# Kernel tuning notes

Hardware: AMD Instinct MI355X
Metric: run time of the kernel (lower is better)

The kernel has to match this reference:

```python
import jax, jax.numpy as jnp
import numpy as np

N_QUBITS = 6
N_LAYERS = 3
FEATURE_DIM = 512
ENC_HIDDEN = max(32, N_QUBITS * 4)  # 32
HEAD_HIDDEN = 128
G, T = 54, 24
DIM = 2 ** N_QUBITS  # 64


def _ry_batched(angles):
    # angles: [B] -> batched RY matrices [B, 2, 2] (complex64)
    c = jnp.cos(angles * 0.5)
    s = jnp.sin(angles * 0.5)
    U = jnp.stack([jnp.stack([c, -s], -1), jnp.stack([s, c], -1)], -2)
    return U.astype(jnp.complex64)


def _rot(phi, theta, omega):
    # PennyLane Rot = RZ(omega) RY(theta) RZ(phi); returns [2, 2] complex64
    c = jnp.cos(theta * 0.5).astype(jnp.complex64)
    s = jnp.sin(theta * 0.5).astype(jnp.complex64)
    ep = jnp.exp(-0.5j * (phi + omega).astype(jnp.complex64))  # e^{-i(phi+omega)/2}
    em = jnp.exp(-0.5j * (phi - omega).astype(jnp.complex64))  # e^{-i(phi-omega)/2}
    u00 = ep * c
    u01 = -jnp.conj(em) * s
    u10 = em * s
    u11 = jnp.conj(ep) * c
    return jnp.stack([jnp.stack([u00, u01]), jnp.stack([u10, u11])])


def _apply_1q_batched(state, U, q):
    # state: [B, 2^n]; U: [B, 2, 2] (per-sample gate, e.g. data-encoding RY)
    B = state.shape[0]
    st = state.reshape(B, 2 ** q, 2, -1)
    st = jnp.einsum('bij,bljr->blir', U, st)
    return st.reshape(B, -1)


def _apply_1q(state, U, q):
    # state: [B, 2^n]; U: [2, 2] shared across batch (trainable Rot)
    B = state.shape[0]
    st = state.reshape(B, 2 ** q, 2, -1)
    st = jnp.einsum('ij,bljr->blir', U, st)
    return st.reshape(B, -1)


def _apply_cnot(state, c, t):
    # state: [B, 2^n]; flip target axis where control bit == 1
    B = state.shape[0]
    st = state.reshape((B,) + (2,) * N_QUBITS)
    ax_c, ax_t = 1 + c, 1 + t
    s0 = jnp.take(st, 0, axis=ax_c)
    s1 = jnp.take(st, 1, axis=ax_c)
    s1 = jnp.flip(s1, axis=ax_t if ax_t < ax_c else ax_t - 1)
    st = jnp.stack([s0, s1], axis=ax_c)
    return st.reshape(B, -1)


def _expvals_z(state):
    # <Z_q> for every qubit: [B, n]
    B = state.shape[0]
    probs = (state.real ** 2 + state.imag ** 2).reshape((B,) + (2,) * N_QUBITS)
    outs = []
    for q in range(N_QUBITS):
        axes = tuple(i for i in range(1, N_QUBITS + 1) if i != q + 1)
        p = probs.sum(axes)  # [B, 2]
        outs.append(p[:, 0] - p[:, 1])
    return jnp.stack(outs, -1)


def _circuit(angles, q_weights):
    # angles: [B, n_qubits] float32; q_weights: [L, n, 3]
    B = angles.shape[0]
    state = jnp.zeros((B, DIM), jnp.complex64).at[:, 0].set(1.0)
    for layer in range(N_LAYERS):
        # data_reuploading=True -> re-encode every layer
        for q in range(N_QUBITS):
            state = _apply_1q_batched(state, _ry_batched(angles[:, q]), q)
        for q in range(N_QUBITS):
            w = q_weights[layer, q]
            state = _apply_1q(state, _rot(w[0], w[1], w[2]), q)
        for q in range(0, N_QUBITS - 1, 2):
            state = _apply_cnot(state, q, q + 1)
        for q in range(1, N_QUBITS - 1, 2):
            state = _apply_cnot(state, q, q + 1)
        state = _apply_cnot(state, N_QUBITS - 1, 0)  # n_qubits > 2
    return _expvals_z(state)


def setup_inputs() -> dict:
    key = jax.random.key(0)
    ks = jax.random.split(key, 10)
    B = 32768
    return {
        'x': jax.random.normal(ks[0], (B, FEATURE_DIM), jnp.float32),
        'enc_w1': 0.05 * jax.random.normal(ks[1], (FEATURE_DIM, ENC_HIDDEN), jnp.float32),
        'enc_b1': jnp.zeros((ENC_HIDDEN,), jnp.float32),
        'enc_w2': 0.05 * jax.random.normal(ks[2], (ENC_HIDDEN, N_QUBITS), jnp.float32),
        'enc_b2': jnp.zeros((N_QUBITS,), jnp.float32),
        'q_weights': 0.01 * jax.random.normal(ks[3], (N_LAYERS, N_QUBITS, 3), jnp.float32),
        'head_w1': 0.1 * jax.random.normal(ks[4], (N_QUBITS, HEAD_HIDDEN), jnp.float32),
        'head_b1': jnp.zeros((HEAD_HIDDEN,), jnp.float32),
        'head_w2': 0.05 * jax.random.normal(ks[5], (HEAD_HIDDEN, G * T), jnp.float32),
        'head_b2': jnp.zeros((G * T,), jnp.float32),
    }


def reference(x, enc_w1, enc_b1, enc_w2, enc_b2, q_weights,
              head_w1, head_b1, head_w2, head_b2):
    # classical encoder -> angles [B, n_qubits]
    h = jnp.tanh(x @ enc_w1 + enc_b1)
    angles = h @ enc_w2 + enc_b2
    # batched state-vector PQC simulation
    z = _circuit(angles, q_weights).astype(jnp.float32)  # [B, n_qubits]
    # classical head (dropout is identity in eval)
    g = jax.nn.relu(z @ head_w1 + head_b1)
    logits = g @ head_w2 + head_b2
    return logits.reshape(-1, G, T)
```

## Files before the change

kernel.cpp:

```cpp
#include <hip/hip_runtime.h>

typedef __bf16 bf16x8 __attribute__((ext_vector_type(8)));
typedef float floatx4 __attribute__((ext_vector_type(4)));
typedef unsigned short ushort8 __attribute__((ext_vector_type(8)));

__device__ __forceinline__ unsigned short f2bf(float f) {
    unsigned u = __float_as_uint(f);
    u += 0x7fffu + ((u >> 16) & 1u);
    return (unsigned short)(u >> 16);
}

__global__ __launch_bounds__(256) void prep_kernel(
    const float* __restrict__ w2, const float* __restrict__ qw,
    unsigned short* __restrict__ w2t, float* __restrict__ umat) {
    int t = blockIdx.x * 256 + threadIdx.x;
    if (t < 18) {
        float phi = qw[t * 3], theta = qw[t * 3 + 1], omega = qw[t * 3 + 2];
        float c = cosf(0.5f * theta), s = sinf(0.5f * theta);
        float po = 0.5f * (phi + omega), pm = 0.5f * (phi - omega);
        float epr = cosf(po), epi = -sinf(po);
        float emr = cosf(pm), emi = -sinf(pm);
        float* u = umat + t * 8;
        u[0] = epr * c;  u[1] = epi * c;
        u[2] = -emr * s; u[3] = emi * s;
        u[4] = emr * s;  u[5] = emi * s;
        u[6] = epr * c;  u[7] = -epi * c;
    }
    int nn = t >> 4;
    int kc = (t & 15) * 8;
    if (nn < 1296) {
        ushort8 pk;
#pragma unroll
        for (int j = 0; j < 8; ++j) pk[j] = f2bf(w2[(size_t)(kc + j) * 1296 + nn]);
        *(ushort8*)(w2t + (size_t)nn * 128 + kc) = pk;
    }
}

__global__ __launch_bounds__(256) void enc_kernel(
    const float* __restrict__ x, const float* __restrict__ w1,
    const float* __restrict__ b1, const float* __restrict__ w2,
    const float* __restrict__ b2, float* __restrict__ angles) {
    __shared__ float part[4][64][33];
    __shared__ float hsh[64][33];
    int lane = threadIdx.x & 63;
    int wave = threadIdx.x >> 6;
    int swave = __builtin_amdgcn_readfirstlane(wave);
    size_t row = (size_t)blockIdx.x * 64 + lane;
    const float2* x2 = (const float2*)(x + row * 512 + swave * 128);
    const float* wseg = w1 + swave * 128 * 32;

    float acc[32];
#pragma unroll
    for (int j = 0; j < 32; ++j) acc[j] = 0.f;

#pragma clang loop unroll(disable)
    for (int k2 = 0; k2 < 64; ++k2) {
        float2 xv = x2[k2];
        const float* wr = wseg + k2 * 64;
#pragma unroll
        for (int j = 0; j < 32; ++j) acc[j] = fmaf(wr[j], xv.x, acc[j]);
#pragma unroll
        for (int j = 0; j < 32; ++j) acc[j] = fmaf(wr[32 + j], xv.y, acc[j]);
    }
#pragma unroll
    for (int j = 0; j < 32; ++j) part[wave][lane][j] = acc[j];
    __syncthreads();

    int rl = threadIdx.x & 63;
    int jg = (threadIdx.x >> 6) * 8;
#pragma unroll
    for (int jj = 0; jj < 8; ++jj) {
        int j = jg + jj;
        float v = part[0][rl][j] + part[1][rl][j] + part[2][rl][j] + part[3][rl][j] + b1[j];
        hsh[rl][j] = tanhf(v);
    }
    __syncthreads();

    if (threadIdx.x < 64) {
        float h[32];
#pragma unroll
        for (int j = 0; j < 32; ++j) h[j] = hsh[threadIdx.x][j];
#pragma unroll
        for (int q = 0; q < 6; ++q) {
            float a = b2[q];
#pragma unroll
            for (int j = 0; j < 32; ++j) a = fmaf(h[j], w2[j * 6 + q], a);
            angles[((size_t)blockIdx.x * 64 + threadIdx.x) * 6 + q] = a;
        }
    }
}

template <int ST>
__device__ __forceinline__ void apply_g(float* sr, float* si,
    float m00r, float m00i, float m01r, float m01i,
    float m10r, float m10i, float m11r, float m11i) {
#pragma unroll
    for (int i = 0; i < 64; ++i) {
        if ((i & ST) == 0) {
            int i1 = i + ST;
            float r0 = sr[i], u0 = si[i], r1 = sr[i1], u1 = si[i1];
            sr[i]  = m00r * r0 - m00i * u0 + m01r * r1 - m01i * u1;
            si[i]  = m00r * u0 + m00i * r0 + m01r * u1 + m01i * r1;
            sr[i1] = m10r * r0 - m10i * u0 + m11r * r1 - m11i * u1;
            si[i1] = m10r * u0 + m10i * r0 + m11r * u1 + m11i * r1;
        }
    }
}

template <int CB, int TB>
__device__ __forceinline__ void cnot_g(float* sr, float* si) {
#pragma unroll
    for (int i = 0; i < 64; ++i) {
        if ((i & CB) && !(i & TB)) {
            int i1 = i + TB;
            float tr = sr[i]; sr[i] = sr[i1]; sr[i1] = tr;
            float ti = si[i]; si[i] = si[i1]; si[i1] = ti;
        }
    }
}

__global__ __launch_bounds__(64) void quantum_kernel(
    const float* __restrict__ angles, const float* __restrict__ umat,
    const float* __restrict__ hw1, const float* __restrict__ hb1,
    unsigned short* __restrict__ g) {
    int s = blockIdx.x * 64 + threadIdx.x;
    float ca[6], sa[6];
#pragma unroll
    for (int q = 0; q < 6; ++q) {
        float a = 0.5f * angles[(size_t)s * 6 + q];
        ca[q] = cosf(a);
        sa[q] = sinf(a);
    }
    float sr[64], si[64];
#pragma unroll
    for (int i = 0; i < 64; ++i) { sr[i] = 0.f; si[i] = 0.f; }
    sr[0] = 1.f;

#pragma clang loop unroll(disable)
    for (int layer = 0; layer < 3; ++layer) {
        const float* ub = umat + layer * 48;
#define DOQ(Q, ST) {                                                      \
        const float* u = ub + (Q) * 8;                                    \
        float c = ca[Q], ss = sa[Q];                                      \
        float m00r = u[0] * c + u[2] * ss, m00i = u[1] * c + u[3] * ss;   \
        float m01r = u[2] * c - u[0] * ss, m01i = u[3] * c - u[1] * ss;   \
        float m10r = u[4] * c + u[6] * ss, m10i = u[5] * c + u[7] * ss;   \
        float m11r = u[6] * c - u[4] * ss, m11i = u[7] * c - u[5] * ss;   \
        apply_g<ST>(sr, si, m00r, m00i, m01r, m01i, m10r, m10i, m11r, m11i); }
        DOQ(0, 32) DOQ(1, 16) DOQ(2, 8) DOQ(3, 4) DOQ(4, 2) DOQ(5, 1)
#undef DOQ
        cnot_g<32, 16>(sr, si);
        cnot_g<8, 4>(sr, si);
        cnot_g<2, 1>(sr, si);
        cnot_g<16, 8>(sr, si);
        cnot_g<4, 2>(sr, si);
        cnot_g<1, 32>(sr, si);
    }

    float z[6] = {0.f, 0.f, 0.f, 0.f, 0.f, 0.f};
#pragma unroll
    for (int i = 0; i < 64; ++i) {
        float p = sr[i] * sr[i] + si[i] * si[i];
        z[0] += (i & 32) ? -p : p;
        z[1] += (i & 16) ? -p : p;
        z[2] += (i & 8)  ? -p : p;
        z[3] += (i & 4)  ? -p : p;
        z[4] += (i & 2)  ? -p : p;
        z[5] += (i & 1)  ? -p : p;
    }

    unsigned short* gp = g + (size_t)s * 128;
#pragma unroll 2
    for (int j0 = 0; j0 < 128; j0 += 8) {
        ushort8 pk;
#pragma unroll
        for (int jj = 0; jj < 8; ++jj) {
            int j = j0 + jj;
            float a = hb1[j];
#pragma unroll
            for (int q = 0; q < 6; ++q) a = fmaf(z[q], hw1[q * 128 + j], a);
            a = fmaxf(a, 0.f);
            pk[jj] = f2bf(a);
        }
        *(ushort8*)(gp + j0) = pk;
    }
}

__global__ __launch_bounds__(256) void head_gemm(
    const unsigned short* __restrict__ g, const unsigned short* __restrict__ w2t,
    const float* __restrict__ b2, float* __restrict__ out) {
    int lane = threadIdx.x & 63;
    int task = blockIdx.x * 4 + (threadIdx.x >> 6);
    int m = task / 27;
    int n = task - m * 27;
    int row0 = m * 64, col0 = n * 48;
    int l15 = lane & 15, quad = lane >> 4;

    const unsigned short* ap = w2t + (size_t)(col0 + l15) * 128 + quad * 8;
    const unsigned short* bp = g + (size_t)(row0 + l15) * 128 + quad * 8;

    floatx4 acc[12];
#pragma unroll
    for (int i = 0; i < 12; ++i) acc[i] = (floatx4)0.f;

#pragma unroll
    for (int ks = 0; ks < 4; ++ks) {
        bf16x8 af[3], bf[4];
#pragma unroll
        for (int t = 0; t < 3; ++t) af[t] = *(const bf16x8*)(ap + (size_t)t * 16 * 128 + ks * 32);
#pragma unroll
        for (int sub = 0; sub < 4; ++sub) bf[sub] = *(const bf16x8*)(bp + (size_t)sub * 16 * 128 + ks * 32);
#pragma unroll
        for (int t = 0; t < 3; ++t)
#pragma unroll
            for (int sub = 0; sub < 4; ++sub)
                acc[t * 4 + sub] = __builtin_amdgcn_mfma_f32_16x16x32_bf16(af[t], bf[sub], acc[t * 4 + sub], 0, 0, 0);
    }

#pragma unroll
    for (int t = 0; t < 3; ++t) {
        const float* bb = b2 + col0 + t * 16 + quad * 4;
        floatx4 bias = { bb[0], bb[1], bb[2], bb[3] };
#pragma unroll
        for (int sub = 0; sub < 4; ++sub) {
            floatx4 v = acc[t * 4 + sub] + bias;
            floatx4* dst = (floatx4*)(out + (size_t)(row0 + sub * 16 + l15) * 1296 + col0 + t * 16 + quad * 4);
            __builtin_nontemporal_store(v, dst);
        }
    }
}

extern "C" void kernel_launch(void* const* d_in, const int* in_sizes, int n_in,
                              void* d_out, int out_size, void* d_ws, size_t ws_size,
                              hipStream_t stream) {
    const float* x   = (const float*)d_in[0];
    const float* ew1 = (const float*)d_in[1];
    const float* eb1 = (const float*)d_in[2];
    const float* ew2 = (const float*)d_in[3];
    const float* eb2 = (const float*)d_in[4];
    const float* qw  = (const float*)d_in[5];
    const float* hw1 = (const float*)d_in[6];
    const float* hb1 = (const float*)d_in[7];
    const float* hw2 = (const float*)d_in[8];
    const float* hb2 = (const float*)d_in[9];
    float* out = (float*)d_out;

    char* ws = (char*)d_ws;
    unsigned short* g   = (unsigned short*)(ws);
    unsigned short* w2t = (unsigned short*)(ws + 8388608);
    float* angles       = (float*)(ws + 8720384);
    float* umat         = (float*)(ws + 9506816);

    prep_kernel<<<dim3(81), dim3(256), 0, stream>>>(hw2, qw, w2t, umat);
    enc_kernel<<<dim3(512), dim3(256), 0, stream>>>(x, ew1, eb1, ew2, eb2, angles);
    quantum_kernel<<<dim3(512), dim3(64), 0, stream>>>(angles, umat, hw1, hb1, g);
    head_gemm<<<dim3(3456), dim3(256), 0, stream>>>(g, w2t, hb2, out);
}
```

Before: 318.6 us.

## Fuse prep, encoder and quantum kernels into one front kernel

```diff
diff --git a/kernel.cpp b/kernel.cpp
--- a/kernel.cpp
+++ b/kernel.cpp
@@ -8,86 +8,6 @@
     unsigned u = __float_as_uint(f);
     u += 0x7fffu + ((u >> 16) & 1u);
     return (unsigned short)(u >> 16);
-}
-
-__global__ __launch_bounds__(256) void prep_kernel(
-    const float* __restrict__ w2, const float* __restrict__ qw,
-    unsigned short* __restrict__ w2t, float* __restrict__ umat) {
-    int t = blockIdx.x * 256 + threadIdx.x;
-    if (t < 18) {
-        float phi = qw[t * 3], theta = qw[t * 3 + 1], omega = qw[t * 3 + 2];
-        float c = cosf(0.5f * theta), s = sinf(0.5f * theta);
-        float po = 0.5f * (phi + omega), pm = 0.5f * (phi - omega);
-        float epr = cosf(po), epi = -sinf(po);
-        float emr = cosf(pm), emi = -sinf(pm);
-        float* u = umat + t * 8;
-        u[0] = epr * c;  u[1] = epi * c;
-        u[2] = -emr * s; u[3] = emi * s;
-        u[4] = emr * s;  u[5] = emi * s;
-        u[6] = epr * c;  u[7] = -epi * c;
-    }
-    int nn = t >> 4;
-    int kc = (t & 15) * 8;
-    if (nn < 1296) {
-        ushort8 pk;
-#pragma unroll
-        for (int j = 0; j < 8; ++j) pk[j] = f2bf(w2[(size_t)(kc + j) * 1296 + nn]);
-        *(ushort8*)(w2t + (size_t)nn * 128 + kc) = pk;
-    }
-}
-
-__global__ __launch_bounds__(256) void enc_kernel(
-    const float* __restrict__ x, const float* __restrict__ w1,
-    const float* __restrict__ b1, const float* __restrict__ w2,
-    const float* __restrict__ b2, float* __restrict__ angles) {
-    __shared__ float part[4][64][33];
-    __shared__ float hsh[64][33];
-    int lane = threadIdx.x & 63;
-    int wave = threadIdx.x >> 6;
-    int swave = __builtin_amdgcn_readfirstlane(wave);
-    size_t row = (size_t)blockIdx.x * 64 + lane;
-    const float2* x2 = (const float2*)(x + row * 512 + swave * 128);
-    const float* wseg = w1 + swave * 128 * 32;
-
-    float acc[32];
-#pragma unroll
-    for (int j = 0; j < 32; ++j) acc[j] = 0.f;
-
-#pragma clang loop unroll(disable)
-    for (int k2 = 0; k2 < 64; ++k2) {
-        float2 xv = x2[k2];
-        const float* wr = wseg + k2 * 64;
-#pragma unroll
-        for (int j = 0; j < 32; ++j) acc[j] = fmaf(wr[j], xv.x, acc[j]);
-#pragma unroll
-        for (int j = 0; j < 32; ++j) acc[j] = fmaf(wr[32 + j], xv.y, acc[j]);
-    }
-#pragma unroll
-    for (int j = 0; j < 32; ++j) part[wave][lane][j] = acc[j];
-    __syncthreads();
-
-    int rl = threadIdx.x & 63;
-    int jg = (threadIdx.x >> 6) * 8;
-#pragma unroll
-    for (int jj = 0; jj < 8; ++jj) {
-        int j = jg + jj;
-        float v = part[0][rl][j] + part[1][rl][j] + part[2][rl][j] + part[3][rl][j] + b1[j];
-        hsh[rl][j] = tanhf(v);
-    }
-    __syncthreads();
-
-    if (threadIdx.x < 64) {
-        float h[32];
-#pragma unroll
-        for (int j = 0; j < 32; ++j) h[j] = hsh[threadIdx.x][j];
-#pragma unroll
-        for (int q = 0; q < 6; ++q) {
-            float a = b2[q];
-#pragma unroll
-            for (int j = 0; j < 32; ++j) a = fmaf(h[j], w2[j * 6 + q], a);
-            angles[((size_t)blockIdx.x * 64 + threadIdx.x) * 6 + q] = a;
-        }
-    }
 }
 
 template <int ST>
@@ -119,18 +39,95 @@
     }
 }
 
-__global__ __launch_bounds__(64) void quantum_kernel(
-    const float* __restrict__ angles, const float* __restrict__ umat,
+__global__ __launch_bounds__(256) void fused_front(
+    const float* __restrict__ x, const float* __restrict__ w1,
+    const float* __restrict__ b1, const float* __restrict__ w2,
+    const float* __restrict__ b2, const float* __restrict__ qw,
     const float* __restrict__ hw1, const float* __restrict__ hb1,
-    unsigned short* __restrict__ g) {
-    int s = blockIdx.x * 64 + threadIdx.x;
+    const float* __restrict__ hw2,
+    unsigned short* __restrict__ w2t, unsigned short* __restrict__ g) {
+
+    if (blockIdx.x >= 512) {
+        int t = (blockIdx.x - 512) * 256 + threadIdx.x;
+        int nn = t >> 4;
+        int kc = (t & 15) * 8;
+        if (nn < 1296) {
+            ushort8 pk;
+#pragma unroll
+            for (int j = 0; j < 8; ++j) pk[j] = f2bf(hw2[(size_t)(kc + j) * 1296 + nn]);
+            *(ushort8*)(w2t + (size_t)nn * 128 + kc) = pk;
+        }
+        return;
+    }
+
+    __shared__ float part[4][64][33];
+    __shared__ float hsh[64][33];
+    __shared__ float umat_s[144];
+
+    if (threadIdx.x < 18) {
+        int t = threadIdx.x;
+        float phi = qw[t * 3], theta = qw[t * 3 + 1], omega = qw[t * 3 + 2];
+        float c = cosf(0.5f * theta), s = sinf(0.5f * theta);
+        float po = 0.5f * (phi + omega), pm = 0.5f * (phi - omega);
+        float epr = cosf(po), epi = -sinf(po);
+        float emr = cosf(pm), emi = -sinf(pm);
+        float* u = umat_s + t * 8;
+        u[0] = epr * c;  u[1] = epi * c;
+        u[2] = -emr * s; u[3] = emi * s;
+        u[4] = emr * s;  u[5] = emi * s;
+        u[6] = epr * c;  u[7] = -epi * c;
+    }
+
+    int lane = threadIdx.x & 63;
+    int wave = threadIdx.x >> 6;
+    int swave = __builtin_amdgcn_readfirstlane(wave);
+    size_t row = (size_t)blockIdx.x * 64 + lane;
+    const float2* x2 = (const float2*)(x + row * 512 + swave * 128);
+    const float* wseg = w1 + swave * 128 * 32;
+
+    float acc[32];
+#pragma unroll
+    for (int j = 0; j < 32; ++j) acc[j] = 0.f;
+
+#pragma clang loop unroll(disable)
+    for (int k2 = 0; k2 < 64; ++k2) {
+        float2 xv = x2[k2];
+        const float* wr = wseg + k2 * 64;
+#pragma unroll
+        for (int j = 0; j < 32; ++j) acc[j] = fmaf(wr[j], xv.x, acc[j]);
+#pragma unroll
+        for (int j = 0; j < 32; ++j) acc[j] = fmaf(wr[32 + j], xv.y, acc[j]);
+    }
+#pragma unroll
+    for (int j = 0; j < 32; ++j) part[wave][lane][j] = acc[j];
+    __syncthreads();
+
+    int rl = threadIdx.x & 63;
+    int jg = (threadIdx.x >> 6) * 8;
+#pragma unroll
+    for (int jj = 0; jj < 8; ++jj) {
+        int j = jg + jj;
+        float v = part[0][rl][j] + part[1][rl][j] + part[2][rl][j] + part[3][rl][j] + b1[j];
+        hsh[rl][j] = tanhf(v);
+    }
+    __syncthreads();
+
+    if (threadIdx.x >= 64) return;
+
+    float h[32];
+#pragma unroll
+    for (int j = 0; j < 32; ++j) h[j] = hsh[threadIdx.x][j];
     float ca[6], sa[6];
 #pragma unroll
     for (int q = 0; q < 6; ++q) {
-        float a = 0.5f * angles[(size_t)s * 6 + q];
+        float a = b2[q];
+#pragma unroll
+        for (int j = 0; j < 32; ++j) a = fmaf(h[j], w2[j * 6 + q], a);
+        a = 0.5f * a;
         ca[q] = cosf(a);
         sa[q] = sinf(a);
     }
+
     float sr[64], si[64];
 #pragma unroll
     for (int i = 0; i < 64; ++i) { sr[i] = 0.f; si[i] = 0.f; }
@@ -138,7 +135,7 @@
 
 #pragma clang loop unroll(disable)
     for (int layer = 0; layer < 3; ++layer) {
-        const float* ub = umat + layer * 48;
+        const float* ub = umat_s + layer * 48;
 #define DOQ(Q, ST) {                                                      \
         const float* u = ub + (Q) * 8;                                    \
         float c = ca[Q], ss = sa[Q];                                      \
@@ -169,6 +166,7 @@
         z[5] += (i & 1)  ? -p : p;
     }
 
+    int s = blockIdx.x * 64 + threadIdx.x;
     unsigned short* gp = g + (size_t)s * 128;
 #pragma unroll 2
     for (int j0 = 0; j0 < 128; j0 += 8) {
@@ -248,11 +246,7 @@
     char* ws = (char*)d_ws;
     unsigned short* g   = (unsigned short*)(ws);
     unsigned short* w2t = (unsigned short*)(ws + 8388608);
-    float* angles       = (float*)(ws + 8720384);
-    float* umat         = (float*)(ws + 9506816);
-
-    prep_kernel<<<dim3(81), dim3(256), 0, stream>>>(hw2, qw, w2t, umat);
-    enc_kernel<<<dim3(512), dim3(256), 0, stream>>>(x, ew1, eb1, ew2, eb2, angles);
-    quantum_kernel<<<dim3(512), dim3(64), 0, stream>>>(angles, umat, hw1, hb1, g);
+
+    fused_front<<<dim3(593), dim3(256), 0, stream>>>(x, ew1, eb1, ew2, eb2, qw, hw1, hb1, hw2, w2t, g);
     head_gemm<<<dim3(3456), dim3(256), 0, stream>>>(g, w2t, hb2, out);
 }
```

New measurement: 350.9 us. +10.2%, slower.

## Fuse head hidden layer into head GEMM via LDS, drop g round-trip

Applied to the files above, without the earlier changes.

```diff
diff --git a/kernel.cpp b/kernel.cpp
--- a/kernel.cpp
+++ b/kernel.cpp
@@ -10,10 +10,10 @@
     return (unsigned short)(u >> 16);
 }
 
-__global__ __launch_bounds__(256) void prep_kernel(
-    const float* __restrict__ w2, const float* __restrict__ qw,
+__global__ __launch_bounds__(512) void prep_kernel(
+    const float* __restrict__ hw2, const float* __restrict__ qw,
     unsigned short* __restrict__ w2t, float* __restrict__ umat) {
-    int t = blockIdx.x * 256 + threadIdx.x;
+    int t = blockIdx.x * 512 + threadIdx.x;
     if (t < 18) {
         float phi = qw[t * 3], theta = qw[t * 3 + 1], omega = qw[t * 3 + 2];
         float c = cosf(0.5f * theta), s = sinf(0.5f * theta);
@@ -31,7 +31,7 @@
     if (nn < 1296) {
         ushort8 pk;
 #pragma unroll
-        for (int j = 0; j < 8; ++j) pk[j] = f2bf(w2[(size_t)(kc + j) * 1296 + nn]);
+        for (int j = 0; j < 8; ++j) pk[j] = f2bf(hw2[(size_t)(kc + j) * 1296 + nn]);
         *(ushort8*)(w2t + (size_t)nn * 128 + kc) = pk;
     }
 }
@@ -121,8 +121,7 @@
 
 __global__ __launch_bounds__(64) void quantum_kernel(
     const float* __restrict__ angles, const float* __restrict__ umat,
-    const float* __restrict__ hw1, const float* __restrict__ hb1,
-    unsigned short* __restrict__ g) {
+    float* __restrict__ z) {
     int s = blockIdx.x * 64 + threadIdx.x;
     float ca[6], sa[6];
 #pragma unroll
@@ -157,75 +156,80 @@
         cnot_g<1, 32>(sr, si);
     }
 
-    float z[6] = {0.f, 0.f, 0.f, 0.f, 0.f, 0.f};
+    float zz[6] = {0.f, 0.f, 0.f, 0.f, 0.f, 0.f};
 #pragma unroll
     for (int i = 0; i < 64; ++i) {
         float p = sr[i] * sr[i] + si[i] * si[i];
-        z[0] += (i & 32) ? -p : p;
-        z[1] += (i & 16) ? -p : p;
-        z[2] += (i & 8)  ? -p : p;
-        z[3] += (i & 4)  ? -p : p;
-        z[4] += (i & 2)  ? -p : p;
-        z[5] += (i & 1)  ? -p : p;
-    }
-
-    unsigned short* gp = g + (size_t)s * 128;
-#pragma unroll 2
-    for (int j0 = 0; j0 < 128; j0 += 8) {
+        zz[0] += (i & 32) ? -p : p;
+        zz[1] += (i & 16) ? -p : p;
+        zz[2] += (i & 8)  ? -p : p;
+        zz[3] += (i & 4)  ? -p : p;
+        zz[4] += (i & 2)  ? -p : p;
+        zz[5] += (i & 1)  ? -p : p;
+    }
+#pragma unroll
+    for (int q = 0; q < 6; ++q) z[(size_t)s * 6 + q] = zz[q];
+}
+
+__global__ __launch_bounds__(256) void head_gemm(
+    const float* __restrict__ z, const unsigned short* __restrict__ w2t,
+    const float* __restrict__ hw1, const float* __restrict__ hb1,
+    const float* __restrict__ b2, float* __restrict__ out) {
+    __shared__ unsigned short gl[16 * 128];
+    __shared__ float zsh[16][6];
+
+    int tid = threadIdx.x;
+    int row0 = blockIdx.x * 16;
+
+    if (tid < 96) zsh[tid / 6][tid % 6] = z[(size_t)row0 * 6 + tid];
+    __syncthreads();
+
+    {
+        int r = tid >> 4;
+        int u = tid & 15;
+        int j0 = u * 8;
+        float zr[6];
+#pragma unroll
+        for (int q = 0; q < 6; ++q) zr[q] = zsh[r][q];
         ushort8 pk;
 #pragma unroll
         for (int jj = 0; jj < 8; ++jj) {
             int j = j0 + jj;
             float a = hb1[j];
 #pragma unroll
-            for (int q = 0; q < 6; ++q) a = fmaf(z[q], hw1[q * 128 + j], a);
+            for (int q = 0; q < 6; ++q) a = fmaf(zr[q], hw1[q * 128 + j], a);
             a = fmaxf(a, 0.f);
             pk[jj] = f2bf(a);
         }
-        *(ushort8*)(gp + j0) = pk;
-    }
-}
-
-__global__ __launch_bounds__(256) void head_gemm(
-    const unsigned short* __restrict__ g, const unsigned short* __restrict__ w2t,
-    const float* __restrict__ b2, float* __restrict__ out) {
-    int lane = threadIdx.x & 63;
-    int task = blockIdx.x * 4 + (threadIdx.x >> 6);
-    int m = task / 27;
-    int n = task - m * 27;
-    int row0 = m * 64, col0 = n * 48;
+        int us = u ^ (r & 7);
+        *(ushort8*)(gl + r * 128 + us * 8) = pk;
+    }
+    __syncthreads();
+
+    int lane = tid & 63, wv = tid >> 6;
     int l15 = lane & 15, quad = lane >> 4;
-
-    const unsigned short* ap = w2t + (size_t)(col0 + l15) * 128 + quad * 8;
-    const unsigned short* bp = g + (size_t)(row0 + l15) * 128 + quad * 8;
-
-    floatx4 acc[12];
-#pragma unroll
-    for (int i = 0; i < 12; ++i) acc[i] = (floatx4)0.f;
-
-#pragma unroll
-    for (int ks = 0; ks < 4; ++ks) {
-        bf16x8 af[3], bf[4];
-#pragma unroll
-        for (int t = 0; t < 3; ++t) af[t] = *(const bf16x8*)(ap + (size_t)t * 16 * 128 + ks * 32);
-#pragma unroll
-        for (int sub = 0; sub < 4; ++sub) bf[sub] = *(const bf16x8*)(bp + (size_t)sub * 16 * 128 + ks * 32);
-#pragma unroll
-        for (int t = 0; t < 3; ++t)
-#pragma unroll
-            for (int sub = 0; sub < 4; ++sub)
-                acc[t * 4 + sub] = __builtin_amdgcn_mfma_f32_16x16x32_bf16(af[t], bf[sub], acc[t * 4 + sub], 0, 0, 0);
-    }
-
-#pragma unroll
-    for (int t = 0; t < 3; ++t) {
-        const float* bb = b2 + col0 + t * 16 + quad * 4;
-        floatx4 bias = { bb[0], bb[1], bb[2], bb[3] };
-#pragma unroll
-        for (int sub = 0; sub < 4; ++sub) {
-            floatx4 v = acc[t * 4 + sub] + bias;
-            floatx4* dst = (floatx4*)(out + (size_t)(row0 + sub * 16 + l15) * 1296 + col0 + t * 16 + quad * 4);
-            __builtin_nontemporal_store(v, dst);
+    int a7 = l15 & 7;
+
+    for (int n = wv; n < 27; n += 4) {
+        int col0 = n * 48;
+#pragma unroll
+        for (int t = 0; t < 3; ++t) {
+            const unsigned short* ap =
+                w2t + (size_t)(col0 + t * 16 + l15) * 128 + quad * 8;
+
+            floatx4 acc = (floatx4)0.f;
+#pragma unroll
+            for (int ks = 0; ks < 4; ++ks) {
+                bf16x8 af = *(const bf16x8*)(ap + ks * 32);
+                int u = (quad + 4 * ks) ^ a7;
+                bf16x8 bf = *(const bf16x8*)(gl + l15 * 128 + u * 8);
+                acc = __builtin_amdgcn_mfma_f32_16x16x32_bf16(af, bf, acc, 0, 0, 0);
+            }
+
+            const float* bb = b2 + col0 + t * 16 + quad * 4;
+            floatx4 bias = { bb[0], bb[1], bb[2], bb[3] };
+            floatx4 v = acc + bias;
+            *(floatx4*)(out + (size_t)(row0 + l15) * 1296 + col0 + t * 16 + quad * 4) = v;
         }
     }
 }
@@ -246,13 +250,13 @@
     float* out = (float*)d_out;
 
     char* ws = (char*)d_ws;
-    unsigned short* g   = (unsigned short*)(ws);
-    unsigned short* w2t = (unsigned short*)(ws + 8388608);
-    float* angles       = (float*)(ws + 8720384);
-    float* umat         = (float*)(ws + 9506816);
-
-    prep_kernel<<<dim3(81), dim3(256), 0, stream>>>(hw2, qw, w2t, umat);
+    unsigned short* w2t = (unsigned short*)(ws);
+    float* umat   = (float*)(ws + 331776);
+    float* angles = (float*)(ws + 332352);
+    float* z      = (float*)(ws + 1118784);
+
+    prep_kernel<<<dim3(41), dim3(512), 0, stream>>>(hw2, qw, w2t, umat);
     enc_kernel<<<dim3(512), dim3(256), 0, stream>>>(x, ew1, eb1, ew2, eb2, angles);
-    quantum_kernel<<<dim3(512), dim3(64), 0, stream>>>(angles, umat, hw1, hb1, g);
-    head_gemm<<<dim3(3456), dim3(256), 0, stream>>>(g, w2t, hb2, out);
-}
+    quantum_kernel<<<dim3(512), dim3(64), 0, stream>>>(angles, umat, z);
+    head_gemm<<<dim3(2048), dim3(256), 0, stream>>>(z, w2t, hw1, hb1, hb2, out);
+}
```

Result: slower. 361.2 us (+13.4%).
